# Optimization experiments

Hardware: AMD Instinct MI355X
Metric: run time of the kernel (lower is better)

## Reference

```python
import jax, jax.numpy as jnp
import numpy as np

SHIFT_RANGE = 8
LOSS_WEIGHT = 10.0
EPS = 1e-12


def _l2_normalize_rows(x):
    # matches F.normalize(x) on flattened rows: x / max(||x||_2, 1e-12)
    n = jnp.sqrt(jnp.sum(x * x, axis=1, keepdims=True))
    return x / jnp.maximum(n, EPS)


def _similarity(grd_feature, sat_feature):
    N, C, Hk, Wk = grd_feature.shape
    grd = _l2_normalize_rows(grd_feature.reshape(N, -1)).reshape(N, C, Hk, Wk)

    S = SHIFT_RANGE
    sat = jnp.pad(sat_feature, ((0, 0), (0, 0), (S, S), (S, S)))
    M, _, Hi, Wi = sat.shape
    sat = _l2_normalize_rows(sat.reshape(M, -1)).reshape(M, C, Hi, Wi)

    # all-pairs valid cross-correlation: corr[m,n,i,j] = sum_{c,h,w} sat[m,c,i+h,j+w]*grd[n,c,h,w]
    # lax.conv is cross-correlation, identical to the groups=N conv2d trick in torch.
    corr = jax.lax.conv_general_dilated(
        sat, grd, window_strides=(1, 1), padding='VALID',
        dimension_numbers=('NCHW', 'OIHW', 'NCHW'))  # [M, N, 2S+1, 2S+1]

    # avg_pool2d(sat^2, (Hk,Wk), stride=1, divisor_override=1) summed over channels
    energy = jnp.sum(sat * sat, axis=1)  # [M, Hi, Wi]
    partical = jax.lax.reduce_window(
        energy, 0.0, jax.lax.add, (1, Hk, Wk), (1, 1, 1), 'VALID')[:, None]  # [M,1,2S+1,2S+1]

    corr = corr / jnp.maximum(jnp.sqrt(partical), EPS)  # uncertainty = 1
    sim = jnp.max(corr, axis=(2, 3))  # [M, N]
    return sim


def _loss(sat_feature, grd_feature):
    B = grd_feature.shape[0]
    sim = _similarity(grd_feature, sat_feature)
    dist = 2.0 - 2.0 * sim  # [B, B], rows=sat, cols=grd
    pos = jnp.diagonal(dist)  # [B]
    pair_n = B * (B - 1)

    # log(1 + exp(x)) == softplus(x)
    loss_g2s = jnp.sum(jax.nn.softplus((pos[None, :] - dist) * LOSS_WEIGHT)) / pair_n
    loss_s2g = jnp.sum(jax.nn.softplus((pos[:, None] - dist) * LOSS_WEIGHT)) / pair_n
    loss = (loss_g2s + loss_s2g) / 2.0

    real_pos_dist_avg = jnp.mean(pos)
    pred_pos_dist_avg = jnp.mean(jnp.min(dist, axis=1))
    return 10.0 * loss, real_pos_dist_avg, pred_pos_dist_avg


def setup_inputs() -> dict:
    key = jax.random.key(0)
    k1, k2 = jax.random.split(key)
    sat_feature = jax.random.normal(k1, (16, 128, 64, 64), dtype=jnp.float32)
    grd_feature = jax.random.normal(k2, (16, 128, 64, 64), dtype=jnp.float32)
    return {"sat_feature": sat_feature, "grd_feature": grd_feature}


def reference(sat_feature, grd_feature):
    return _loss(sat_feature, grd_feature)
```

## Files before the change

### kernel.cpp

```cpp
#include <hip/hip_runtime.h>
#include <math.h>

#define CCH 128
#define HH 64
#define WW 64
#define SHD 17
#define NSHIFT (SHD*SHD)

#define OFF_KEY    0
#define OFF_NPART  256
#define OFF_EPART  8448
#define OFF_SCALE  532736
#define OFF_SATP_B 2162688
#define SATP_SLICE_U16 (64*80*16*16)
#define OFF_GRDB_B (OFF_SATP_B + 8*SATP_SLICE_U16*2)
#define GRD_SLICE_U16 (64*64*16*16)
#define OFF_PART_B (OFF_GRDB_B + 8*GRD_SLICE_U16*2)
#define NBLK_CORR 1088

typedef __bf16 bf16x8 __attribute__((ext_vector_type(8)));
typedef float floatx4 __attribute__((ext_vector_type(4)));
typedef unsigned short ushort8 __attribute__((ext_vector_type(8)));

#define AS1 __attribute__((address_space(1)))
#define AS3 __attribute__((address_space(3)))

__device__ inline unsigned short f2bf(float f) {
    unsigned x = __float_as_uint(f);
    unsigned r = x + 0x7FFFu + ((x >> 16) & 1u);
    return (unsigned short)(r >> 16);
}

__global__ __launch_bounds__(256) void k_prep(const float* __restrict__ sat,
                                              const float* __restrict__ grd,
                                              float* __restrict__ ws) {
    __shared__ unsigned short tile[64 * 256];
    __shared__ float nred[16];
    int b = blockIdx.x;
    int tensor = b >> 9, h = (b >> 3) & 63, csl = b & 7;
    const float* src = tensor ? grd : sat;
    unsigned short* dstS = (unsigned short*)((char*)ws + OFF_SATP_B);
    unsigned short* dstG = (unsigned short*)((char*)ws + OFF_GRDB_B);
    int t = threadIdx.x;
    int n = t >> 4, wq = t & 15;

    float en0 = 0.f, en1 = 0.f, en2 = 0.f, en3 = 0.f;
    const float* base = src + ((size_t)(n * CCH + csl * 16) * 4096) + h * 64 + wq * 4;
    int w0 = wq * 4;
    #pragma unroll
    for (int c = 0; c < 16; ++c) {
        float4 v = *(const float4*)(base + (size_t)c * 4096);
        en0 = fmaf(v.x, v.x, en0); en1 = fmaf(v.y, v.y, en1);
        en2 = fmaf(v.z, v.z, en2); en3 = fmaf(v.w, v.w, en3);
        tile[(w0 + 0) * 256 + ((n + w0 + 0) & 15) * 16 + c] = f2bf(v.x);
        tile[(w0 + 1) * 256 + ((n + w0 + 1) & 15) * 16 + c] = f2bf(v.y);
        tile[(w0 + 2) * 256 + ((n + w0 + 2) & 15) * 16 + c] = f2bf(v.z);
        tile[(w0 + 3) * 256 + ((n + w0 + 3) & 15) * 16 + c] = f2bf(v.w);
    }

    if (tensor == 0) {
        float* eg = ws + OFF_EPART + (size_t)csl * 65536 + ((size_t)n * 64 + h) * 64 + w0;
        *(float4*)eg = make_float4(en0, en1, en2, en3);
    } else {
        float s = en0 + en1 + en2 + en3;
        #pragma unroll
        for (int off = 8; off; off >>= 1) s += __shfl_xor(s, off);
        if (wq == 0) nred[n] = s;
    }

    __syncthreads();
    if (tensor == 1 && t < 16)
        ws[OFF_NPART + (size_t)(h * 8 + csl) * 16 + t] = nred[t];

    unsigned short* dst = tensor
        ? dstG + (size_t)csl * GRD_SLICE_U16 + (size_t)h * 16384
        : dstS + (size_t)csl * SATP_SLICE_U16 + ((size_t)h * 80 + 8) * 256;
    #pragma unroll
    for (int i = 0; i < 8; ++i) {
        int o = i * 256 + t;
        int w = o >> 5, nn = (o >> 1) & 15, c8 = o & 1;
        ushort8 val = *(ushort8*)&tile[w * 256 + ((nn + w) & 15) * 16 + c8 * 8];
        *(ushort8*)&dst[(size_t)o * 8] = val;
    }
    if (tensor == 0) {
        ushort8 z = (ushort8)0;
        #pragma unroll
        for (int i = 0; i < 2; ++i) {
            int o = i * 256 + t;
            int slot = o >> 5, wi = o & 31;
            int ps = slot < 8 ? slot : slot + 64;
            *(ushort8*)&dstS[(size_t)csl * SATP_SLICE_U16 +
                             ((size_t)h * 80 + ps) * 256 + wi * 8] = z;
        }
    }
}

__global__ __launch_bounds__(320) void k_scale(float* __restrict__ ws) {
    __shared__ float E[64 * 64];
    __shared__ float R[64 * 17];
    int m = blockIdx.x;
    int t = threadIdx.x;
    float* scale = ws + OFF_SCALE + (size_t)m * NSHIFT;
    if (t < 16) ((unsigned*)ws)[OFF_KEY + m * 16 + t] = 0u;
    const float* ep = ws + OFF_EPART + (size_t)m * 4096;
    for (int i = t; i < 4096; i += 320) {
        float s = 0.f;
        #pragma unroll
        for (int csl = 0; csl < 8; ++csl) s += ep[(size_t)csl * 65536 + i];
        E[i] = s;
    }
    __syncthreads();
    for (int i = t; i < 64 * 17; i += 320) {
        int y = i / 17, j = i % 17;
        int x0 = max(0, j - 8), x1 = min(64, j + 56);
        float s = 0.f;
        for (int x = x0; x < x1; ++x) s += E[y * 64 + x];
        R[i] = s;
    }
    __syncthreads();
    for (int idx = t; idx < NSHIFT; idx += 320) {
        int ii = idx / 17, j = idx % 17;
        int y0 = max(0, ii - 8), y1 = min(64, ii + 56);
        float s = 0.f;
        for (int y = y0; y < y1; ++y) s += R[y * 17 + j];
        scale[idx] = 1.f / fmaxf(sqrtf(s), 1e-12f);
    }
}

__global__ __launch_bounds__(256, 2) void k_corr(const unsigned short* __restrict__ satp,
                                                 const unsigned short* __restrict__ grdb,
                                                 float* __restrict__ part) {
    __shared__ alignas(16) unsigned char smem[81920];
    int b = blockIdx.x;
    int csl = b & 7;
    int r2  = b >> 3;
    int dyi = r2 % 17;
    int hq  = r2 / 17;
    int h0  = hq * 8;
    int t = threadIdx.x;
    int wv = t >> 6, l = t & 63;
    int m16 = l & 15, q = l >> 4, jl = q >> 1, c8 = q & 1;
    int wbase = wv * 16;

    const unsigned short* sats = satp + (size_t)csl * SATP_SLICE_U16;
    const unsigned short* grds = grdb + (size_t)csl * GRD_SLICE_U16;
    const unsigned short* goff = grds + ((wbase + jl) * 16 + m16) * 16 + c8 * 8;
    int hl = max(0, 8 - dyi - h0), hu = min(8, 72 - dyi - h0);

    floatx4 acc[17];
    #pragma unroll
    for (int d = 0; d < 17; ++d) acc[d] = (floatx4)0.f;

    #define STAGE(hs, p)                                                            \
        do {                                                                        \
            _Pragma("unroll")                                                       \
            for (int i_ = 0; i_ < 10; ++i_) {                                       \
                const unsigned short* g_ = sats + (size_t)(hs) * 20480              \
                                         + wv * 5120 + i_ * 512 + l * 8;            \
                __builtin_amdgcn_global_load_lds((AS1 void*)(unsigned short*)g_,    \
                    (AS3 void*)(smem + (p) * 40960 + wv * 10240 + i_ * 1024 + l * 16), \
                    16, 0, 0);                                                      \
            }                                                                       \
        } while (0)

    if (hl < hu) {
        int hs0 = h0 + hl + dyi - 8;
        STAGE(hs0, 0);
        bf16x8 Bc[8], Bn[8];
        #pragma unroll
        for (int bi = 0; bi < 8; ++bi)
            Bc[bi] = *(const bf16x8*)(goff + (size_t)(h0 + hl) * 16384 + bi * 512);

        for (int hh = hl; hh < hu; ++hh) {
            __syncthreads();
            int p = (hh - hl) & 1;
            if (hh + 1 < hu) {
                STAGE(hs0 + (hh - hl) + 1, p ^ 1);
                #pragma unroll
                for (int bi = 0; bi < 8; ++bi)
                    Bn[bi] = *(const bf16x8*)(goff + (size_t)(h0 + hh + 1) * 16384 + bi * 512);
            }
            const unsigned char* aptr = smem + p * 40960 + jl * 512 + m16 * 32 + c8 * 16;
            bf16x8 Ar[4];
            #pragma unroll
            for (int i = 0; i < 4; ++i)
                Ar[i] = *(const bf16x8*)(aptr + (size_t)(wbase + i) * 512);
            #pragma unroll
            for (int wo = 0; wo < 31; ++wo) {
                bf16x8 A = Ar[wo & 3];
                if (wo + 4 < 31)
                    Ar[wo & 3] = *(const bf16x8*)(aptr + (size_t)(wbase + wo + 4) * 512);
                #pragma unroll
                for (int bi = 0; bi < 8; ++bi) {
                    const int dxi = wo - 2 * bi;
                    if (dxi >= 0 && dxi <= 16)
                        acc[dxi] = __builtin_amdgcn_mfma_f32_16x16x32_bf16(A, Bc[bi], acc[dxi], 0, 0, 0);
                }
            }
            #pragma unroll
            for (int bi = 0; bi < 8; ++bi) Bc[bi] = Bn[bi];
        }
    }
    #undef STAGE

    __syncthreads();
    float* red = (float*)smem;
    #pragma unroll
    for (int dxi = 0; dxi < 17; ++dxi)
        #pragma unroll
        for (int r = 0; r < 4; ++r)
            red[(size_t)(wv * 68 + dxi * 4 + r) * 64 + l] = acc[dxi][r];
    __syncthreads();
    float* pw = part + (size_t)b * 4352;
    #pragma unroll
    for (int k = 0; k < 17; ++k) {
        int row = wv * 17 + k;
        float s = red[(size_t)(0 * 68 + row) * 64 + l]
                + red[(size_t)(1 * 68 + row) * 64 + l]
                + red[(size_t)(2 * 68 + row) * 64 + l]
                + red[(size_t)(3 * 68 + row) * 64 + l];
        pw[(size_t)row * 64 + l] = s;
    }
}

__global__ void k_reduce(const float* __restrict__ part, float* __restrict__ ws) {
    int b = blockIdx.x;
    int dyi = b / 17, dxi = b % 17;
    int t = threadIdx.x;
    int l = t & 63, r = t >> 6;
    size_t eo = (size_t)(dxi * 4 + r) * 64 + l;
    float s = 0.f;
    for (int hq = 0; hq < 8; ++hq) {
        #pragma unroll
        for (int csl = 0; csl < 8; ++csl) {
            size_t blk = (size_t)((hq * 17 + dyi) * 8 + csl);
            s += part[blk * 4352 + eo];
        }
    }
    int n = l & 15, q = l >> 4, m = q * 4 + r;
    float val = s * ws[OFF_SCALE + m * NSHIFT + dyi * 17 + dxi];
    int iv = __float_as_int(val);
    unsigned key = (iv >= 0) ? ((unsigned)iv | 0x80000000u) : (unsigned)(~iv);
    atomicMax((unsigned*)ws + OFF_KEY + m * 16 + n, key);
}

__global__ void k_final(const float* __restrict__ ws, float* __restrict__ out) {
    const unsigned* keys = (const unsigned*)ws + OFF_KEY;
    __shared__ float dist_s[256];
    __shared__ float pos_s[16];
    __shared__ float red[256];
    __shared__ float minv[16];
    __shared__ float norms_s[16];
    int t = threadIdx.x;
    int m = t >> 4, n = t & 15;

    if (t < 16) {
        float s = 0.f;
        const float* np = ws + OFF_NPART + t;
        #pragma unroll 8
        for (int j = 0; j < 512; ++j) s += np[(size_t)j * 16];
        norms_s[t] = s;
    }
    __syncthreads();

    unsigned u = keys[t];
    int iv = (u & 0x80000000u) ? (int)(u & 0x7fffffffu) : ~(int)u;
    float best = __int_as_float(iv);
    float Ng  = sqrtf(norms_s[n]);
    float sim = best / fmaxf(Ng, 1e-12f);
    float d   = 2.f - 2.f * sim;
    dist_s[t] = d;
    if (m == n) pos_s[m] = d;
    __syncthreads();

    float x1 = (pos_s[n] - d) * 10.f;
    float x2 = (pos_s[m] - d) * 10.f;
    float sp1 = x1 > 20.f ? x1 : log1pf(expf(x1));
    float sp2 = x2 > 20.f ? x2 : log1pf(expf(x2));
    red[t] = sp1 + sp2;
    __syncthreads();
    for (int off = 128; off; off >>= 1) {
        if (t < off) red[t] += red[t + off];
        __syncthreads();
    }
    if (t < 16) {
        float mv = 1e30f;
        for (int nn = 0; nn < 16; ++nn) mv = fminf(mv, dist_s[t * 16 + nn]);
        minv[t] = mv;
    }
    __syncthreads();
    if (t == 0) {
        float psum = 0.f, msum = 0.f;
        for (int qq = 0; qq < 16; ++qq) { psum += pos_s[qq]; msum += minv[qq]; }
        out[0] = red[0] / 48.f;
        out[1] = psum / 16.f;
        out[2] = msum / 16.f;
    }
}

extern "C" void kernel_launch(void* const* d_in, const int* in_sizes, int n_in,
                              void* d_out, int out_size, void* d_ws, size_t ws_size,
                              hipStream_t stream) {
    const float* sat = (const float*)d_in[0];
    const float* grd = (const float*)d_in[1];
    float* out = (float*)d_out;
    float* ws  = (float*)d_ws;
    const unsigned short* satp = (const unsigned short*)((char*)d_ws + OFF_SATP_B);
    const unsigned short* grdb = (const unsigned short*)((char*)d_ws + OFF_GRDB_B);
    float* part = (float*)((char*)d_ws + OFF_PART_B);

    k_prep  <<<1024,      256, 0, stream>>>(sat, grd, ws);
    k_scale <<<16,        320, 0, stream>>>(ws);
    k_corr  <<<NBLK_CORR, 256, 0, stream>>>(satp, grdb, part);
    k_reduce<<<NSHIFT,    256, 0, stream>>>(part, ws);
    k_final <<<1,         256, 0, stream>>>(ws, out);
}
```

Baseline: 205.0 us.

## Fold scale and final kernels into corr and reduce to cut launches

The k_scale work now runs in 16 extra blocks appended to the k_corr grid. The k_final loss computation moves into the last-finishing k_reduce block, found with an atomic counter, which removes two kernel launches and their gaps. The per-image norms are precomputed in those scale blocks. The A-operand register prefetch depth in the MFMA inner loop drops from 4 to 1, which lowers register pressure but may expose LDS latency.

```diff
diff --git a/kernel.cpp b/kernel.cpp
--- a/kernel.cpp
+++ b/kernel.cpp
@@ -11,12 +11,14 @@
 #define OFF_NPART  256
 #define OFF_EPART  8448
 #define OFF_SCALE  532736
+#define OFF_NORMS  537360
+#define OFF_CNT    537376
 #define OFF_SATP_B 2162688
 #define SATP_SLICE_U16 (64*80*16*16)
 #define OFF_GRDB_B (OFF_SATP_B + 8*SATP_SLICE_U16*2)
 #define GRD_SLICE_U16 (64*64*16*16)
 #define OFF_PART_B (OFF_GRDB_B + 8*GRD_SLICE_U16*2)
-#define NBLK_CORR 1088
+#define NBLK_CORR 1104
 
 typedef __bf16 bf16x8 __attribute__((ext_vector_type(8)));
 typedef float floatx4 __attribute__((ext_vector_type(4)));
@@ -95,49 +97,61 @@
     }
 }
 
-__global__ __launch_bounds__(320) void k_scale(float* __restrict__ ws) {
-    __shared__ float E[64 * 64];
-    __shared__ float R[64 * 17];
-    int m = blockIdx.x;
-    int t = threadIdx.x;
-    float* scale = ws + OFF_SCALE + (size_t)m * NSHIFT;
-    if (t < 16) ((unsigned*)ws)[OFF_KEY + m * 16 + t] = 0u;
-    const float* ep = ws + OFF_EPART + (size_t)m * 4096;
-    for (int i = t; i < 4096; i += 320) {
-        float s = 0.f;
-        #pragma unroll
-        for (int csl = 0; csl < 8; ++csl) s += ep[(size_t)csl * 65536 + i];
-        E[i] = s;
-    }
-    __syncthreads();
-    for (int i = t; i < 64 * 17; i += 320) {
-        int y = i / 17, j = i % 17;
-        int x0 = max(0, j - 8), x1 = min(64, j + 56);
-        float s = 0.f;
-        for (int x = x0; x < x1; ++x) s += E[y * 64 + x];
-        R[i] = s;
-    }
-    __syncthreads();
-    for (int idx = t; idx < NSHIFT; idx += 320) {
-        int ii = idx / 17, j = idx % 17;
-        int y0 = max(0, ii - 8), y1 = min(64, ii + 56);
-        float s = 0.f;
-        for (int y = y0; y < y1; ++y) s += R[y * 17 + j];
-        scale[idx] = 1.f / fmaxf(sqrtf(s), 1e-12f);
-    }
-}
-
 __global__ __launch_bounds__(256, 2) void k_corr(const unsigned short* __restrict__ satp,
                                                  const unsigned short* __restrict__ grdb,
-                                                 float* __restrict__ part) {
+                                                 float* __restrict__ part,
+                                                 float* __restrict__ ws) {
     __shared__ alignas(16) unsigned char smem[81920];
     int b = blockIdx.x;
+    int t = threadIdx.x;
+
+    if (b >= 1088) {
+        int m = b - 1088;
+        float* E  = (float*)smem;
+        float* R  = E + 4096;
+        float* nr = R + 1088;
+        if (t < 16) ((unsigned*)ws)[OFF_KEY + m * 16 + t] = 0u;
+        if (m == 0 && t == 0) ((unsigned*)ws)[OFF_CNT] = 0u;
+        float s = 0.f;
+        for (int j = t; j < 512; j += 256) s += ws[OFF_NPART + (size_t)j * 16 + m];
+        nr[t] = s; __syncthreads();
+        for (int off = 128; off; off >>= 1) {
+            if (t < off) nr[t] += nr[t + off];
+            __syncthreads();
+        }
+        if (t == 0) ws[OFF_NORMS + m] = nr[0];
+        const float* ep = ws + OFF_EPART + (size_t)m * 4096;
+        for (int i = t; i < 4096; i += 256) {
+            float e = 0.f;
+            #pragma unroll
+            for (int c = 0; c < 8; ++c) e += ep[(size_t)c * 65536 + i];
+            E[i] = e;
+        }
+        __syncthreads();
+        for (int i = t; i < 64 * 17; i += 256) {
+            int y = i / 17, j = i % 17;
+            int x0 = max(0, j - 8), x1 = min(64, j + 56);
+            float e = 0.f;
+            for (int x = x0; x < x1; ++x) e += E[y * 64 + x];
+            R[i] = e;
+        }
+        __syncthreads();
+        float* scale = ws + OFF_SCALE + (size_t)m * NSHIFT;
+        for (int idx = t; idx < NSHIFT; idx += 256) {
+            int ii = idx / 17, j = idx % 17;
+            int y0 = max(0, ii - 8), y1 = min(64, ii + 56);
+            float e = 0.f;
+            for (int y = y0; y < y1; ++y) e += R[y * 17 + j];
+            scale[idx] = 1.f / fmaxf(sqrtf(e), 1e-12f);
+        }
+        return;
+    }
+
     int csl = b & 7;
     int r2  = b >> 3;
     int dyi = r2 % 17;
     int hq  = r2 / 17;
     int h0  = hq * 8;
-    int t = threadIdx.x;
     int wv = t >> 6, l = t & 63;
     int m16 = l & 15, q = l >> 4, jl = q >> 1, c8 = q & 1;
     int wbase = wv * 16;
@@ -181,21 +195,18 @@
                     Bn[bi] = *(const bf16x8*)(goff + (size_t)(h0 + hh + 1) * 16384 + bi * 512);
             }
             const unsigned char* aptr = smem + p * 40960 + jl * 512 + m16 * 32 + c8 * 16;
-            bf16x8 Ar[4];
-            #pragma unroll
-            for (int i = 0; i < 4; ++i)
-                Ar[i] = *(const bf16x8*)(aptr + (size_t)(wbase + i) * 512);
+            bf16x8 A = *(const bf16x8*)(aptr + (size_t)wbase * 512);
             #pragma unroll
             for (int wo = 0; wo < 31; ++wo) {
-                bf16x8 A = Ar[wo & 3];
-                if (wo + 4 < 31)
-                    Ar[wo & 3] = *(const bf16x8*)(aptr + (size_t)(wbase + wo + 4) * 512);
+                bf16x8 An = A;
+                if (wo < 30) An = *(const bf16x8*)(aptr + (size_t)(wbase + wo + 1) * 512);
                 #pragma unroll
                 for (int bi = 0; bi < 8; ++bi) {
                     const int dxi = wo - 2 * bi;
                     if (dxi >= 0 && dxi <= 16)
                         acc[dxi] = __builtin_amdgcn_mfma_f32_16x16x32_bf16(A, Bc[bi], acc[dxi], 0, 0, 0);
                 }
+                A = An;
             }
             #pragma unroll
             for (int bi = 0; bi < 8; ++bi) Bc[bi] = Bn[bi];
@@ -223,7 +234,8 @@
     }
 }
 
-__global__ void k_reduce(const float* __restrict__ part, float* __restrict__ ws) {
+__global__ void k_reduce(const float* __restrict__ part, float* __restrict__ ws,
+                         float* __restrict__ out) {
     int b = blockIdx.x;
     int dyi = b / 17, dxi = b % 17;
     int t = threadIdx.x;
@@ -242,57 +254,52 @@
     int iv = __float_as_int(val);
     unsigned key = (iv >= 0) ? ((unsigned)iv | 0x80000000u) : (unsigned)(~iv);
     atomicMax((unsigned*)ws + OFF_KEY + m * 16 + n, key);
-}
-
-__global__ void k_final(const float* __restrict__ ws, float* __restrict__ out) {
-    const unsigned* keys = (const unsigned*)ws + OFF_KEY;
+
+    __shared__ unsigned done;
+    __syncthreads();
+    if (t == 0) {
+        __threadfence();
+        done = atomicAdd((unsigned*)ws + OFF_CNT, 1u);
+    }
+    __syncthreads();
+    if (done != 288) return;
+    __threadfence();
+
     __shared__ float dist_s[256];
     __shared__ float pos_s[16];
-    __shared__ float red[256];
+    __shared__ float red2[256];
     __shared__ float minv[16];
-    __shared__ float norms_s[16];
-    int t = threadIdx.x;
-    int m = t >> 4, n = t & 15;
-
-    if (t < 16) {
-        float s = 0.f;
-        const float* np = ws + OFF_NPART + t;
-        #pragma unroll 8
-        for (int j = 0; j < 512; ++j) s += np[(size_t)j * 16];
-        norms_s[t] = s;
-    }
-    __syncthreads();
-
-    unsigned u = keys[t];
-    int iv = (u & 0x80000000u) ? (int)(u & 0x7fffffffu) : ~(int)u;
-    float best = __int_as_float(iv);
-    float Ng  = sqrtf(norms_s[n]);
+    unsigned u = atomicOr((unsigned*)ws + OFF_KEY + t, 0u);
+    int iv2 = (u & 0x80000000u) ? (int)(u & 0x7fffffffu) : ~(int)u;
+    float best = __int_as_float(iv2);
+    int mm = t >> 4, nn = t & 15;
+    float Ng  = sqrtf(ws[OFF_NORMS + nn]);
     float sim = best / fmaxf(Ng, 1e-12f);
     float d   = 2.f - 2.f * sim;
     dist_s[t] = d;
-    if (m == n) pos_s[m] = d;
-    __syncthreads();
-
-    float x1 = (pos_s[n] - d) * 10.f;
-    float x2 = (pos_s[m] - d) * 10.f;
+    if (mm == nn) pos_s[mm] = d;
+    __syncthreads();
+
+    float x1 = (pos_s[nn] - d) * 10.f;
+    float x2 = (pos_s[mm] - d) * 10.f;
     float sp1 = x1 > 20.f ? x1 : log1pf(expf(x1));
     float sp2 = x2 > 20.f ? x2 : log1pf(expf(x2));
-    red[t] = sp1 + sp2;
+    red2[t] = sp1 + sp2;
     __syncthreads();
     for (int off = 128; off; off >>= 1) {
-        if (t < off) red[t] += red[t + off];
+        if (t < off) red2[t] += red2[t + off];
         __syncthreads();
     }
     if (t < 16) {
         float mv = 1e30f;
-        for (int nn = 0; nn < 16; ++nn) mv = fminf(mv, dist_s[t * 16 + nn]);
+        for (int k = 0; k < 16; ++k) mv = fminf(mv, dist_s[t * 16 + k]);
         minv[t] = mv;
     }
     __syncthreads();
     if (t == 0) {
         float psum = 0.f, msum = 0.f;
         for (int qq = 0; qq < 16; ++qq) { psum += pos_s[qq]; msum += minv[qq]; }
-        out[0] = red[0] / 48.f;
+        out[0] = red2[0] / 48.f;
         out[1] = psum / 16.f;
         out[2] = msum / 16.f;
     }
@@ -310,8 +317,6 @@
     float* part = (float*)((char*)d_ws + OFF_PART_B);
 
     k_prep  <<<1024,      256, 0, stream>>>(sat, grd, ws);
-    k_scale <<<16,        320, 0, stream>>>(ws);
-    k_corr  <<<NBLK_CORR, 256, 0, stream>>>(satp, grdb, part);
-    k_reduce<<<NSHIFT,    256, 0, stream>>>(part, ws);
-    k_final <<<1,         256, 0, stream>>>(ws, out);
-}
+    k_corr  <<<NBLK_CORR, 256, 0, stream>>>(satp, grdb, part, ws);
+    k_reduce<<<NSHIFT,    256, 0, stream>>>(part, ws, out);
+}
```

New measurement: 178.8 us. 12.8% less time.
